# Kernel tuning notes

Hardware: AMD Instinct MI355X
Metric: run time of the kernel (lower is better)

Reference implementation:

```python
import jax, jax.numpy as jnp
import numpy as np

B, D, H, W, C = 4, 8, 16, 16, 512
K_RED = 8
R = C // K_RED          # reduced channels for Q/K
EPS = 1e-3              # keras LayerNormalization default epsilon


def setup_inputs() -> dict:
    key = jax.random.key(0)
    ks = jax.random.split(key, 8)
    s = 0.02
    f32 = jnp.float32
    return {
        "x":  jax.random.normal(ks[0], (B, D, H, W, C), f32),
        # 1x1x1 Conv3D == per-position linear over channels
        "wq": (jax.random.normal(ks[1], (C, R), f32) * s), "bq": jnp.zeros((R,), f32),
        "wk": (jax.random.normal(ks[2], (C, R), f32) * s), "bk": jnp.zeros((R,), f32),
        "wv": (jax.random.normal(ks[3], (C, C), f32) * s), "bv": jnp.zeros((C,), f32),
        "wm": (jax.random.normal(ks[4], (C, C), f32) * s), "bm": jnp.zeros((C,), f32),
        "g1": jnp.ones((C,), f32), "b1": jnp.zeros((C,), f32),
        "g2": jnp.ones((C,), f32), "b2": jnp.zeros((C,), f32),
    }


def _layer_norm(x, g, b):
    m = jnp.mean(x, axis=-1, keepdims=True)
    v = jnp.mean(jnp.square(x - m), axis=-1, keepdims=True)
    return (x - m) * jax.lax.rsqrt(v + EPS) * g + b


def reference(x, wq, bq, wk, bk, wv, bv, wm, bm, g1, b1, g2, b2):
    b, d, h, w, c = x.shape
    f = h * w
    xf = x.reshape(b, d, f, c)                      # [B,D,F,C]
    Q = xf @ wq + bq                                # [B,D,F,R]
    K = xf @ wk + bk                                # [B,D,F,R]
    V = xf @ wv + bv                                # [B,D,F,C]
    # full global scores: [B, D, F, D, F]
    e = jnp.einsum('bifr,bgjr->bifgj', Q, K)
    alphas = jax.nn.softmax(e.reshape(b, d, f, d * f), axis=-1)
    alphas = alphas.reshape(b, d, f, d, f)
    # original einsum 'bdfgh,bdhi->bdfi' sums over key-depth g and uses V at
    # the query depth d; fold the g-sum first, then per-depth F x F matmul.
    a2 = alphas.sum(axis=3)                         # [B,D,F,F]
    attn = jnp.einsum('bdfh,bdhc->bdfc', a2, V)     # [B,D,F,C]
    y1 = _layer_norm(attn + xf, g1, b1)
    y2 = _layer_norm(y1 + jax.nn.relu(y1 @ wm + bm), g2, b2)
    return y2.reshape(b, d, h, w, c)
```

## Files before the change

kernel.cpp:

```cpp
#include <hip/hip_runtime.h>
#include <cstdint>

#define LN_EPS 1e-3f
using u16 = unsigned short;
using u32 = unsigned int;
typedef __attribute__((ext_vector_type(8))) short bh8;
typedef __attribute__((ext_vector_type(4))) float f4;
#define MFMA16(A,B,C) __builtin_amdgcn_mfma_f32_16x16x32_bf16((A),(B),(C),0,0,0)
#define SBAR() __builtin_amdgcn_s_barrier()
#define CFENCE() asm volatile("" ::: "memory")
#define WAITV(N) asm volatile("s_waitcnt vmcnt(" #N ")" ::: "memory")
#define LKBAR() do{ asm volatile("s_waitcnt lgkmcnt(0)" ::: "memory"); \
                    __builtin_amdgcn_s_barrier(); asm volatile("" ::: "memory"); }while(0)

__device__ __forceinline__ u16 bf16r(float f){
    union{float f;u32 u;} c; c.f=f;
    return (u16)((c.u + 0x7fffu + ((c.u>>16)&1u))>>16);
}
__device__ __forceinline__ u32 pk2(float a, float b){
    return (u32)bf16r(a) | ((u32)bf16r(b)<<16);
}
__device__ __forceinline__ void glds16(const void* g, void* l){
    __builtin_amdgcn_global_load_lds(
        (const __attribute__((address_space(1))) u32*)g,
        (__attribute__((address_space(3))) u32*)l, 16, 0, 0);
}

__global__ __launch_bounds__(256) void k0_prep(
    const float* __restrict__ wq, const float* __restrict__ wk,
    const float* __restrict__ wv, const float* __restrict__ wm,
    u16* __restrict__ wqkv_p, u16* __restrict__ wm_p)
{
    const int t = threadIdx.x;
    const int c = t & 15, qn = t >> 4;
    const int quad = qn & 3, ntl = qn >> 2;
    const int blk = blockIdx.x;
    if (blk < 32){
        const int s = blk >> 1, hh = blk & 1;
        const int krow = s*32 + quad*8;
        u16* dst = wqkv_p + (size_t)s*20480;
        #pragma unroll
        for (int i=0;i<5;++i){
            const int nt = hh*20 + i*4 + ntl;
            const int n = nt*16 + c;
            const float* src; int ldw;
            if (n < 64){ src = wq + (size_t)krow*64 + n; ldw = 64; }
            else if (n < 128){ src = wk + (size_t)krow*64 + (n-64); ldw = 64; }
            else { src = wv + (size_t)krow*512 + (n-128); ldw = 512; }
            float v[8];
            #pragma unroll
            for (int j=0;j<8;++j) v[j] = src[(size_t)j*ldw];
            uint4 o; o.x=pk2(v[0],v[1]); o.y=pk2(v[2],v[3]); o.z=pk2(v[4],v[5]); o.w=pk2(v[6],v[7]);
            *(uint4*)&dst[((nt*4+quad)*16 + c)*8] = o;
        }
    } else {
        const int bb = blk - 32;
        const int s = bb >> 1, hh = bb & 1;
        const int krow = s*32 + quad*8;
        u16* dst = wm_p + (size_t)s*16384;
        #pragma unroll
        for (int i=0;i<4;++i){
            const int nt = hh*16 + i*4 + ntl;
            const int n = nt*16 + c;
            const float* src = wm + (size_t)krow*512 + n;
            float v[8];
            #pragma unroll
            for (int j=0;j<8;++j) v[j] = src[(size_t)j*512];
            uint4 o; o.x=pk2(v[0],v[1]); o.y=pk2(v[2],v[3]); o.z=pk2(v[4],v[5]); o.w=pk2(v[6],v[7]);
            *(uint4*)&dst[((nt*4+quad)*16 + c)*8] = o;
        }
    }
}

__global__ __launch_bounds__(512) void k1_qkv(
    const float* __restrict__ x, const float* __restrict__ bq, const float* __restrict__ bk,
    const u16* __restrict__ wqkv_p,
    u16* __restrict__ Qb, u16* __restrict__ Kb, u16* __restrict__ Vb)
{
    __shared__ u16 Asf[16384];
    __shared__ u16 Bs[3][20480];
    const int t = threadIdx.x, w = t>>6, lane = t&63, quad = (lane>>4)&3, c = lane&15;
    const int rg = w>>2, cg = w&3;
    const int rowbase = blockIdx.x << 5;

    #pragma unroll
    for (int i=0;i<5;++i)
        glds16((const char*)wqkv_p + (size_t)w*5120 + i*1024 + lane*16,
               (char*)Bs[0] + w*5120 + i*1024);
    #pragma unroll
    for (int i=0;i<5;++i)
        glds16((const char*)wqkv_p + 40960 + (size_t)w*5120 + i*1024 + lane*16,
               (char*)Bs[1] + w*5120 + i*1024);
    #pragma unroll
    for (int i=0;i<8;++i){
        const int idx = t + (i<<9);
        const int fr = idx >> 7, fc4 = idx & 127;
        float4 xv = *(const float4*)&x[(size_t)(rowbase+fr)*512 + fc4*4];
        uint2 pkv; pkv.x = pk2(xv.x,xv.y); pkv.y = pk2(xv.z,xv.w);
        const int s = fc4 >> 3, qd = (fc4 >> 1) & 3, j0 = (fc4 & 1)*4;
        *(uint2*)&Asf[(fr>>4)*8192 + s*512 + (qd*16 + (fr&15))*8 + j0] = pkv;
    }
    f4 acc[10];
    #pragma unroll
    for (int i=0;i<10;++i) acc[i] = (f4){0.f,0.f,0.f,0.f};
    LKBAR();

    #pragma unroll
    for (int s=0;s<16;++s){
        const u16* Bcur = Bs[s%3];
        bh8 a = *(const bh8*)&Asf[rg*8192 + s*512 + (quad*16+c)*8];
        if (s+2 < 16){
            #pragma unroll
            for (int i=0;i<5;++i)
                glds16((const char*)wqkv_p + (size_t)(s+2)*40960 + (size_t)w*5120 + i*1024 + lane*16,
                       (char*)Bs[(s+2)%3] + w*5120 + i*1024);
            WAITV(10);
        } else if (s+1 < 16){
            WAITV(5);
        } else {
            WAITV(0);
        }
        SBAR(); CFENCE();
        __builtin_amdgcn_s_setprio(1);
        #pragma unroll
        for (int nt2=0;nt2<10;++nt2){
            bh8 bb = *(const bh8*)&Bcur[((cg*10+nt2)*4 + quad)*128 + c*8];
            acc[nt2] = MFMA16(a, bb, acc[nt2]);
        }
        __builtin_amdgcn_s_setprio(0);
        CFENCE(); SBAR();
    }

    const int rt = (blockIdx.x<<1) + rg;
    const int bd = rowbase >> 8;
    const int kloc = (rowbase & 255) + rg*16 + quad*4;
    const int sv = kloc >> 5, kq = (kloc >> 3) & 3, jk0 = kloc & 7;
    #pragma unroll
    for (int nt2=0;nt2<10;++nt2){
        const int colb = cg*160 + nt2*16;
        if (colb < 128){
            const bool isK = (colb >= 64);
            const int r = colb - (isK ? 64 : 0) + c;
            const float bias = isK ? bk[r] : bq[r];
            u16* dstb = (isK ? Kb : Qb) + ((size_t)(rt*2 + (r>>5))*4 + ((r>>3)&3))*128 + (r&7);
            #pragma unroll
            for (int reg=0;reg<4;++reg)
                dstb[(quad*4+reg)*8] = bf16r(acc[nt2][reg] + bias);
        } else {
            const int ntv = (colb - 128) >> 4;
            u16* dstv = Vb + (size_t)bd*131072 + (size_t)sv*16384
                           + (size_t)((ntv*4+kq)*128 + c*8 + jk0);
            ushort4 o;
            o.x = bf16r(acc[nt2][0]); o.y = bf16r(acc[nt2][1]);
            o.z = bf16r(acc[nt2][2]); o.w = bf16r(acc[nt2][3]);
            *(ushort4*)dstv = o;
        }
    }
}

__global__ __launch_bounds__(512) void k234(
    const u16* __restrict__ Qb, const u16* __restrict__ Kb, const u16* __restrict__ Vb,
    const u16* __restrict__ wm_p,
    const float* __restrict__ x, const float* __restrict__ bv,
    const float* __restrict__ g1, const float* __restrict__ b1,
    const float* __restrict__ bm, const float* __restrict__ g2, const float* __restrict__ b2,
    float* __restrict__ out)
{
    __shared__ u16 Bs[3][16384];
    __shared__ u16 y1f[16384];
    __shared__ u16 a2f[8192];
    __shared__ u16 qsf[2048];
    __shared__ float redA[2][4][16], redB[2][4][16];
    const int t = threadIdx.x, w = t>>6, lane = t&63, quad = (lane>>4)&3, c = lane&15;
    const int rg = w>>2, cg = w&3;
    const int bd = blockIdx.x & 31, ftile = blockIdx.x >> 5;
    const int b = bd >> 3;
    const int rowbase = (bd<<8) + (ftile<<5);
    const int rt00 = rowbase >> 4;
    const char* Kbase = (const char*)Kb + (size_t)b*262144;
    const char* Vbase = (const char*)Vb + (size_t)bd*262144;

    if (w < 4) glds16((const char*)Qb + (size_t)rt00*2048 + w*1024 + lane*16,
                      (char*)qsf + w*1024);
    #pragma unroll
    for (int i=0;i<4;++i)
        glds16(Kbase + (size_t)w*4096 + i*1024 + lane*16, (char*)Bs[0] + w*4096 + i*1024);
    #pragma unroll
    for (int i=0;i<4;++i)
        glds16(Kbase + 32768 + (size_t)w*4096 + i*1024 + lane*16, (char*)Bs[1] + w*4096 + i*1024);
    WAITV(8);
    SBAR(); CFENCE();
    bh8 aq0 = *(const bh8*)&qsf[rg*1024 + (quad*16+c)*8];
    bh8 aq1 = *(const bh8*)&qsf[rg*1024 + 512 + (quad*16+c)*8];

    float lp[4] = {0.f,0.f,0.f,0.f};
    float a2r[4][4] = {};
    #pragma unroll
    for (int cc=0; cc<8; ++cc){
        const u16* Bcur = Bs[cc%3];
        if (cc+2 < 8){
            #pragma unroll
            for (int i=0;i<4;++i)
                glds16(Kbase + (size_t)(cc+2)*32768 + (size_t)w*4096 + i*1024 + lane*16,
                       (char*)Bs[(cc+2)%3] + w*4096 + i*1024);
            WAITV(8);
        } else if (cc+1 < 8){
            WAITV(4);
        } else {
            WAITV(0);
        }
        SBAR(); CFENCE();
        __builtin_amdgcn_s_setprio(1);
        f4 sa[4];
        #pragma unroll
        for (int kt=0;kt<4;++kt){
            sa[kt] = (f4){0.f,0.f,0.f,0.f};
            bh8 b0 = *(const bh8*)&Bcur[(cg*4+kt)*1024 + (quad*16+c)*8];
            bh8 bv1= *(const bh8*)&Bcur[(cg*4+kt)*1024 + 512 + (quad*16+c)*8];
            sa[kt] = MFMA16(aq0, b0, sa[kt]);
            sa[kt] = MFMA16(aq1, bv1, sa[kt]);
        }
        __builtin_amdgcn_s_setprio(0);
        #pragma unroll
        for (int kt=0;kt<4;++kt)
            #pragma unroll
            for (int reg=0;reg<4;++reg){
                float e = __expf(sa[kt][reg]);
                lp[reg] += e;
                a2r[reg][kt] += e;
            }
        CFENCE(); SBAR();
    }
    #pragma unroll
    for (int i=0;i<4;++i)
        glds16(Vbase + (size_t)w*4096 + i*1024 + lane*16, (char*)Bs[0] + w*4096 + i*1024);
    #pragma unroll
    for (int i=0;i<4;++i)
        glds16(Vbase + 32768 + (size_t)w*4096 + i*1024 + lane*16, (char*)Bs[1] + w*4096 + i*1024);
    #pragma unroll
    for (int reg=0;reg<4;++reg){
        float v = lp[reg];
        v += __shfl_xor(v,1,64); v += __shfl_xor(v,2,64);
        v += __shfl_xor(v,4,64); v += __shfl_xor(v,8,64);
        lp[reg] = v;
    }
    if (c==0){
        #pragma unroll
        for (int reg=0;reg<4;++reg) redA[rg][cg][quad*4+reg] = lp[reg];
    }
    LKBAR();
    float fac[4];
    #pragma unroll
    for (int reg=0;reg<4;++reg){
        const int q = quad*4+reg;
        fac[reg] = 1.f/(redA[rg][0][q]+redA[rg][1][q]+redA[rg][2][q]+redA[rg][3][q]);
    }
    #pragma unroll
    for (int reg=0;reg<4;++reg)
        #pragma unroll
        for (int kt=0;kt<4;++kt){
            const int jp = cg*64 + kt*16 + c;
            a2f[rg*4096 + (jp>>5)*512 + (((jp>>3)&3)*16 + quad*4+reg)*8 + (jp&7)]
                = bf16r(a2r[reg][kt]*fac[reg]);
        }
    LKBAR();

    f4 cacc[8];
    #pragma unroll
    for (int i=0;i<8;++i) cacc[i] = (f4){0.f,0.f,0.f,0.f};
    #pragma unroll
    for (int s8=0;s8<8;++s8){
        const u16* Bcur = Bs[s8%3];
        bh8 a = *(const bh8*)&a2f[rg*4096 + s8*512 + (quad*16+c)*8];
        if (s8+2 < 8){
            #pragma unroll
            for (int i=0;i<4;++i)
                glds16(Vbase + (size_t)(s8+2)*32768 + (size_t)w*4096 + i*1024 + lane*16,
                       (char*)Bs[(s8+2)%3] + w*4096 + i*1024);
            WAITV(8);
        } else if (s8+1 < 8){
            WAITV(4);
        } else {
            WAITV(0);
        }
        SBAR(); CFENCE();
        __builtin_amdgcn_s_setprio(1);
        #pragma unroll
        for (int nt2=0;nt2<8;++nt2){
            bh8 bb = *(const bh8*)&Bcur[((cg*8+nt2)*4 + quad)*128 + c*8];
            cacc[nt2] = MFMA16(a, bb, cacc[nt2]);
        }
        __builtin_amdgcn_s_setprio(0);
        CFENCE(); SBAR();
    }

    #pragma unroll
    for (int i=0;i<4;++i)
        glds16((const char*)wm_p + (size_t)w*4096 + i*1024 + lane*16,
               (char*)Bs[0] + w*4096 + i*1024);
    #pragma unroll
    for (int i=0;i<4;++i)
        glds16((const char*)wm_p + 32768 + (size_t)w*4096 + i*1024 + lane*16,
               (char*)Bs[1] + w*4096 + i*1024);

    {
        float sv4[4] = {0.f,0.f,0.f,0.f}, qv2[4] = {0.f,0.f,0.f,0.f};
        #pragma unroll
        for (int nt2=0;nt2<8;++nt2){
            const int col = cg*128 + nt2*16 + c;
            const float bvv = bv[col];
            #pragma unroll
            for (int reg=0;reg<4;++reg){
                const int row = rowbase + rg*16 + quad*4 + reg;
                float val = cacc[nt2][reg] + bvv + x[(size_t)row*512 + col];
                cacc[nt2][reg] = val;
                sv4[reg] += val; qv2[reg] = fmaf(val,val,qv2[reg]);
            }
        }
        #pragma unroll
        for (int reg=0;reg<4;++reg){
            float s1=sv4[reg], s2=qv2[reg];
            s1 += __shfl_xor(s1,1,64); s2 += __shfl_xor(s2,1,64);
            s1 += __shfl_xor(s1,2,64); s2 += __shfl_xor(s2,2,64);
            s1 += __shfl_xor(s1,4,64); s2 += __shfl_xor(s2,4,64);
            s1 += __shfl_xor(s1,8,64); s2 += __shfl_xor(s2,8,64);
            sv4[reg]=s1; qv2[reg]=s2;
        }
        if (c==0){
            #pragma unroll
            for (int reg=0;reg<4;++reg){ redA[rg][cg][quad*4+reg]=sv4[reg]; redB[rg][cg][quad*4+reg]=qv2[reg]; }
        }
        LKBAR();
        float mean[4], rstd[4];
        #pragma unroll
        for (int reg=0;reg<4;++reg){
            const int q = quad*4+reg;
            const float S  = redA[rg][0][q]+redA[rg][1][q]+redA[rg][2][q]+redA[rg][3][q];
            const float Q2 = redB[rg][0][q]+redB[rg][1][q]+redB[rg][2][q]+redB[rg][3][q];
            const float m = S*(1.f/512.f);
            mean[reg]=m; rstd[reg]=rsqrtf(Q2*(1.f/512.f) - m*m + LN_EPS);
        }
        #pragma unroll
        for (int nt2=0;nt2<8;++nt2){
            const int col = cg*128 + nt2*16 + c;
            const float gg = g1[col], bb1 = b1[col];
            #pragma unroll
            for (int reg=0;reg<4;++reg){
                float y = (cacc[nt2][reg]-mean[reg])*rstd[reg]*gg + bb1;
                cacc[nt2][reg] = y;
                y1f[rg*8192 + (col>>5)*512 + (((col>>3)&3)*16 + quad*4+reg)*8 + (col&7)] = bf16r(y);
            }
        }
        LKBAR();
    }

    f4 dacc[8];
    #pragma unroll
    for (int i=0;i<8;++i) dacc[i] = (f4){0.f,0.f,0.f,0.f};
    #pragma unroll
    for (int s=0;s<16;++s){
        const u16* Bcur = Bs[s%3];
        bh8 a = *(const bh8*)&y1f[rg*8192 + s*512 + (quad*16+c)*8];
        if (s+2 < 16){
            #pragma unroll
            for (int i=0;i<4;++i)
                glds16((const char*)wm_p + (size_t)(s+2)*32768 + (size_t)w*4096 + i*1024 + lane*16,
                       (char*)Bs[(s+2)%3] + w*4096 + i*1024);
            WAITV(8);
        } else if (s+1 < 16){
            WAITV(4);
        } else {
            WAITV(0);
        }
        SBAR(); CFENCE();
        __builtin_amdgcn_s_setprio(1);
        #pragma unroll
        for (int nt2=0;nt2<8;++nt2){
            bh8 bb = *(const bh8*)&Bcur[((cg*8+nt2)*4 + quad)*128 + c*8];
            dacc[nt2] = MFMA16(a, bb, dacc[nt2]);
        }
        __builtin_amdgcn_s_setprio(0);
        CFENCE(); SBAR();
    }

    {
        float sv4[4] = {0.f,0.f,0.f,0.f}, qv2[4] = {0.f,0.f,0.f,0.f};
        #pragma unroll
        for (int nt2=0;nt2<8;++nt2){
            const int col = cg*128 + nt2*16 + c;
            const float bmv = bm[col];
            #pragma unroll
            for (int reg=0;reg<4;++reg){
                float hh = fmaxf(dacc[nt2][reg]+bmv, 0.f) + cacc[nt2][reg];
                dacc[nt2][reg] = hh;
                sv4[reg] += hh; qv2[reg] = fmaf(hh,hh,qv2[reg]);
            }
        }
        #pragma unroll
        for (int reg=0;reg<4;++reg){
            float s1=sv4[reg], s2=qv2[reg];
            s1 += __shfl_xor(s1,1,64); s2 += __shfl_xor(s2,1,64);
            s1 += __shfl_xor(s1,2,64); s2 += __shfl_xor(s2,2,64);
            s1 += __shfl_xor(s1,4,64); s2 += __shfl_xor(s2,4,64);
            s1 += __shfl_xor(s1,8,64); s2 += __shfl_xor(s2,8,64);
            sv4[reg]=s1; qv2[reg]=s2;
        }
        if (c==0){
            #pragma unroll
            for (int reg=0;reg<4;++reg){ redA[rg][cg][quad*4+reg]=sv4[reg]; redB[rg][cg][quad*4+reg]=qv2[reg]; }
        }
        __syncthreads();
        float mean[4], rstd[4];
        #pragma unroll
        for (int reg=0;reg<4;++reg){
            const int q = quad*4+reg;
            const float S  = redA[rg][0][q]+redA[rg][1][q]+redA[rg][2][q]+redA[rg][3][q];
            const float Q2 = redB[rg][0][q]+redB[rg][1][q]+redB[rg][2][q]+redB[rg][3][q];
            const float m = S*(1.f/512.f);
            mean[reg]=m; rstd[reg]=rsqrtf(Q2*(1.f/512.f) - m*m + LN_EPS);
        }
        #pragma unroll
        for (int nt2=0;nt2<8;++nt2){
            const int col = cg*128 + nt2*16 + c;
            const float gg = g2[col], bb2 = b2[col];
            #pragma unroll
            for (int reg=0;reg<4;++reg){
                const int row = rowbase + rg*16 + quad*4 + reg;
                out[(size_t)row*512 + col] = (dacc[nt2][reg]-mean[reg])*rstd[reg]*gg + bb2;
            }
        }
    }
}

extern "C" void kernel_launch(void* const* d_in, const int* in_sizes, int n_in,
                              void* d_out, int out_size, void* d_ws, size_t ws_size,
                              hipStream_t stream) {
    (void)in_sizes; (void)n_in; (void)out_size; (void)ws_size;
    const float* x  = (const float*)d_in[0];
    const float* wq = (const float*)d_in[1];
    const float* bq = (const float*)d_in[2];
    const float* wk = (const float*)d_in[3];
    const float* bk = (const float*)d_in[4];
    const float* wv = (const float*)d_in[5];
    const float* bv = (const float*)d_in[6];
    const float* wm = (const float*)d_in[7];
    const float* bm = (const float*)d_in[8];
    const float* g1 = (const float*)d_in[9];
    const float* b1 = (const float*)d_in[10];
    const float* g2 = (const float*)d_in[11];
    const float* b2 = (const float*)d_in[12];

    u16* wqkv_p = (u16*)d_ws;
    u16* wm_p   = wqkv_p + 327680;
    u16* Qb     = wm_p   + 262144;
    u16* Kb     = Qb     + 524288;
    u16* Vb     = Kb     + 524288;
    float* outp = (float*)d_out;

    k0_prep<<<64, 256, 0, stream>>>(wq, wk, wv, wm, wqkv_p, wm_p);
    k1_qkv <<<256, 512, 0, stream>>>(x, bq, bk, wqkv_p, Qb, Kb, Vb);
    k234   <<<256, 512, 0, stream>>>(Qb, Kb, Vb, wm_p, x, bv, g1, b1, bm, g2, b2, outp);
}
```

Before: 140.2 us.

## Split k234 into 16-row blocks with double buffering and aliased shared memory

k234 now runs 512 blocks of 256 threads, each handling 16 rows instead of 32. Its triple-buffered shared-memory staging becomes double-buffered, and the q/a2/y1 scratch and reduction buffers are aliased into one region, which cuts LDS per block and should allow more resident blocks. k1's loop is rearranged to wait-then-barrier first and then issue the next prefetch, dropping the trailing barrier. In exchange, each block streams the K/V/Wm tiles for half as many rows, doubling weight and K/V traffic through L2, and the shallower prefetch depth may expose more load latency.

```diff
diff --git a/kernel.cpp b/kernel.cpp
--- a/kernel.cpp
+++ b/kernel.cpp
@@ -107,20 +107,16 @@
 
     #pragma unroll
     for (int s=0;s<16;++s){
-        const u16* Bcur = Bs[s%3];
-        bh8 a = *(const bh8*)&Asf[rg*8192 + s*512 + (quad*16+c)*8];
+        if (s+1 < 16){ WAITV(5); } else { WAITV(0); }
+        SBAR(); CFENCE();
         if (s+2 < 16){
             #pragma unroll
             for (int i=0;i<5;++i)
                 glds16((const char*)wqkv_p + (size_t)(s+2)*40960 + (size_t)w*5120 + i*1024 + lane*16,
                        (char*)Bs[(s+2)%3] + w*5120 + i*1024);
-            WAITV(10);
-        } else if (s+1 < 16){
-            WAITV(5);
-        } else {
-            WAITV(0);
-        }
-        SBAR(); CFENCE();
+        }
+        const u16* Bcur = Bs[s%3];
+        bh8 a = *(const bh8*)&Asf[rg*8192 + s*512 + (quad*16+c)*8];
         __builtin_amdgcn_s_setprio(1);
         #pragma unroll
         for (int nt2=0;nt2<10;++nt2){
@@ -128,7 +124,6 @@
             acc[nt2] = MFMA16(a, bb, acc[nt2]);
         }
         __builtin_amdgcn_s_setprio(0);
-        CFENCE(); SBAR();
     }
 
     const int rt = (blockIdx.x<<1) + rg;
@@ -158,7 +153,7 @@
     }
 }
 
-__global__ __launch_bounds__(512) void k234(
+__global__ __launch_bounds__(256) void k234(
     const u16* __restrict__ Qb, const u16* __restrict__ Kb, const u16* __restrict__ Vb,
     const u16* __restrict__ wm_p,
     const float* __restrict__ x, const float* __restrict__ bv,
@@ -166,50 +161,45 @@
     const float* __restrict__ bm, const float* __restrict__ g2, const float* __restrict__ b2,
     float* __restrict__ out)
 {
-    __shared__ u16 Bs[3][16384];
-    __shared__ u16 y1f[16384];
-    __shared__ u16 a2f[8192];
-    __shared__ u16 qsf[2048];
-    __shared__ float redA[2][4][16], redB[2][4][16];
+    __shared__ u16 Bs[2][16384];
+    __shared__ u16 U[8192];
+    u16* const qsf = U;
+    u16* const a2f = U;
+    u16* const y1f = U;
+    float* const redA = (float*)&U[4096];
+    float* const redB = redA + 64;
     const int t = threadIdx.x, w = t>>6, lane = t&63, quad = (lane>>4)&3, c = lane&15;
-    const int rg = w>>2, cg = w&3;
+    const int cg = w;
     const int bd = blockIdx.x & 31, ftile = blockIdx.x >> 5;
     const int b = bd >> 3;
-    const int rowbase = (bd<<8) + (ftile<<5);
-    const int rt00 = rowbase >> 4;
+    const int rowbase = (bd<<8) + (ftile<<4);
+    const int rt = rowbase >> 4;
     const char* Kbase = (const char*)Kb + (size_t)b*262144;
     const char* Vbase = (const char*)Vb + (size_t)bd*262144;
 
-    if (w < 4) glds16((const char*)Qb + (size_t)rt00*2048 + w*1024 + lane*16,
+    if (w < 2) glds16((const char*)Qb + (size_t)rt*2048 + w*1024 + lane*16,
                       (char*)qsf + w*1024);
     #pragma unroll
-    for (int i=0;i<4;++i)
-        glds16(Kbase + (size_t)w*4096 + i*1024 + lane*16, (char*)Bs[0] + w*4096 + i*1024);
-    #pragma unroll
-    for (int i=0;i<4;++i)
-        glds16(Kbase + 32768 + (size_t)w*4096 + i*1024 + lane*16, (char*)Bs[1] + w*4096 + i*1024);
+    for (int i=0;i<8;++i)
+        glds16(Kbase + (size_t)(w*8+i)*1024 + lane*16, (char*)Bs[0] + (w*8+i)*1024);
     WAITV(8);
     SBAR(); CFENCE();
-    bh8 aq0 = *(const bh8*)&qsf[rg*1024 + (quad*16+c)*8];
-    bh8 aq1 = *(const bh8*)&qsf[rg*1024 + 512 + (quad*16+c)*8];
+    bh8 aq0 = *(const bh8*)&qsf[(quad*16+c)*8];
+    bh8 aq1 = *(const bh8*)&qsf[512 + (quad*16+c)*8];
 
     float lp[4] = {0.f,0.f,0.f,0.f};
     float a2r[4][4] = {};
     #pragma unroll
     for (int cc=0; cc<8; ++cc){
-        const u16* Bcur = Bs[cc%3];
-        if (cc+2 < 8){
-            #pragma unroll
-            for (int i=0;i<4;++i)
-                glds16(Kbase + (size_t)(cc+2)*32768 + (size_t)w*4096 + i*1024 + lane*16,
-                       (char*)Bs[(cc+2)%3] + w*4096 + i*1024);
-            WAITV(8);
-        } else if (cc+1 < 8){
-            WAITV(4);
-        } else {
-            WAITV(0);
-        }
+        WAITV(0);
         SBAR(); CFENCE();
+        if (cc+1 < 8){
+            #pragma unroll
+            for (int i=0;i<8;++i)
+                glds16(Kbase + (size_t)(cc+1)*32768 + (size_t)(w*8+i)*1024 + lane*16,
+                       (char*)Bs[(cc+1)&1] + (w*8+i)*1024);
+        }
+        const u16* Bcur = Bs[cc&1];
         __builtin_amdgcn_s_setprio(1);
         f4 sa[4];
         #pragma unroll
@@ -229,14 +219,10 @@
                 lp[reg] += e;
                 a2r[reg][kt] += e;
             }
-        CFENCE(); SBAR();
-    }
-    #pragma unroll
-    for (int i=0;i<4;++i)
-        glds16(Vbase + (size_t)w*4096 + i*1024 + lane*16, (char*)Bs[0] + w*4096 + i*1024);
-    #pragma unroll
-    for (int i=0;i<4;++i)
-        glds16(Vbase + 32768 + (size_t)w*4096 + i*1024 + lane*16, (char*)Bs[1] + w*4096 + i*1024);
+    }
+    #pragma unroll
+    for (int i=0;i<8;++i)
+        glds16(Vbase + (size_t)(w*8+i)*1024 + lane*16, (char*)Bs[0] + (w*8+i)*1024);
     #pragma unroll
     for (int reg=0;reg<4;++reg){
         float v = lp[reg];
@@ -246,21 +232,24 @@
     }
     if (c==0){
         #pragma unroll
-        for (int reg=0;reg<4;++reg) redA[rg][cg][quad*4+reg] = lp[reg];
+        for (int reg=0;reg<4;++reg) redA[cg*16 + quad*4+reg] = lp[reg];
     }
     LKBAR();
+    #pragma unroll
+    for (int i=0;i<8;++i)
+        glds16(Vbase + 32768 + (size_t)(w*8+i)*1024 + lane*16, (char*)Bs[1] + (w*8+i)*1024);
     float fac[4];
     #pragma unroll
     for (int reg=0;reg<4;++reg){
         const int q = quad*4+reg;
-        fac[reg] = 1.f/(redA[rg][0][q]+redA[rg][1][q]+redA[rg][2][q]+redA[rg][3][q]);
+        fac[reg] = 1.f/(redA[q]+redA[16+q]+redA[32+q]+redA[48+q]);
     }
     #pragma unroll
     for (int reg=0;reg<4;++reg)
         #pragma unroll
         for (int kt=0;kt<4;++kt){
             const int jp = cg*64 + kt*16 + c;
-            a2f[rg*4096 + (jp>>5)*512 + (((jp>>3)&3)*16 + quad*4+reg)*8 + (jp&7)]
+            a2f[(jp>>5)*512 + (((jp>>3)&3)*16 + quad*4+reg)*8 + (jp&7)]
                 = bf16r(a2r[reg][kt]*fac[reg]);
         }
     LKBAR();
@@ -270,20 +259,16 @@
     for (int i=0;i<8;++i) cacc[i] = (f4){0.f,0.f,0.f,0.f};
     #pragma unroll
     for (int s8=0;s8<8;++s8){
-        const u16* Bcur = Bs[s8%3];
-        bh8 a = *(const bh8*)&a2f[rg*4096 + s8*512 + (quad*16+c)*8];
-        if (s8+2 < 8){
-            #pragma unroll
-            for (int i=0;i<4;++i)
-                glds16(Vbase + (size_t)(s8+2)*32768 + (size_t)w*4096 + i*1024 + lane*16,
-                       (char*)Bs[(s8+2)%3] + w*4096 + i*1024);
-            WAITV(8);
-        } else if (s8+1 < 8){
-            WAITV(4);
-        } else {
-            WAITV(0);
-        }
+        if (s8==0){ WAITV(8); } else { WAITV(0); }
         SBAR(); CFENCE();
+        if (s8>=1 && s8+1<8){
+            #pragma unroll
+            for (int i=0;i<8;++i)
+                glds16(Vbase + (size_t)(s8+1)*32768 + (size_t)(w*8+i)*1024 + lane*16,
+                       (char*)Bs[(s8+1)&1] + (w*8+i)*1024);
+        }
+        const u16* Bcur = Bs[s8&1];
+        bh8 a = *(const bh8*)&a2f[s8*512 + (quad*16+c)*8];
         __builtin_amdgcn_s_setprio(1);
         #pragma unroll
         for (int nt2=0;nt2<8;++nt2){
@@ -291,17 +276,11 @@
             cacc[nt2] = MFMA16(a, bb, cacc[nt2]);
         }
         __builtin_amdgcn_s_setprio(0);
-        CFENCE(); SBAR();
-    }
-
-    #pragma unroll
-    for (int i=0;i<4;++i)
-        glds16((const char*)wm_p + (size_t)w*4096 + i*1024 + lane*16,
-               (char*)Bs[0] + w*4096 + i*1024);
-    #pragma unroll
-    for (int i=0;i<4;++i)
-        glds16((const char*)wm_p + 32768 + (size_t)w*4096 + i*1024 + lane*16,
-               (char*)Bs[1] + w*4096 + i*1024);
+    }
+    #pragma unroll
+    for (int i=0;i<8;++i)
+        glds16((const char*)wm_p + (size_t)(w*8+i)*1024 + lane*16,
+               (char*)Bs[0] + (w*8+i)*1024);
 
     {
         float sv4[4] = {0.f,0.f,0.f,0.f}, qv2[4] = {0.f,0.f,0.f,0.f};
@@ -311,7 +290,7 @@
             const float bvv = bv[col];
             #pragma unroll
             for (int reg=0;reg<4;++reg){
-                const int row = rowbase + rg*16 + quad*4 + reg;
+                const int row = rowbase + quad*4 + reg;
                 float val = cacc[nt2][reg] + bvv + x[(size_t)row*512 + col];
                 cacc[nt2][reg] = val;
                 sv4[reg] += val; qv2[reg] = fmaf(val,val,qv2[reg]);
@@ -328,18 +307,23 @@
         }
         if (c==0){
             #pragma unroll
-            for (int reg=0;reg<4;++reg){ redA[rg][cg][quad*4+reg]=sv4[reg]; redB[rg][cg][quad*4+reg]=qv2[reg]; }
+            for (int reg=0;reg<4;++reg){ redA[cg*16+quad*4+reg]=sv4[reg]; redB[cg*16+quad*4+reg]=qv2[reg]; }
         }
         LKBAR();
+        #pragma unroll
+        for (int i=0;i<8;++i)
+            glds16((const char*)wm_p + 32768 + (size_t)(w*8+i)*1024 + lane*16,
+                   (char*)Bs[1] + (w*8+i)*1024);
         float mean[4], rstd[4];
         #pragma unroll
         for (int reg=0;reg<4;++reg){
             const int q = quad*4+reg;
-            const float S  = redA[rg][0][q]+redA[rg][1][q]+redA[rg][2][q]+redA[rg][3][q];
-            const float Q2 = redB[rg][0][q]+redB[rg][1][q]+redB[rg][2][q]+redB[rg][3][q];
+            const float S  = redA[q]+redA[16+q]+redA[32+q]+redA[48+q];
+            const float Q2 = redB[q]+redB[16+q]+redB[32+q]+redB[48+q];
             const float m = S*(1.f/512.f);
             mean[reg]=m; rstd[reg]=rsqrtf(Q2*(1.f/512.f) - m*m + LN_EPS);
         }
+        SBAR(); CFENCE();
         #pragma unroll
         for (int nt2=0;nt2<8;++nt2){
             const int col = cg*128 + nt2*16 + c;
@@ -348,7 +332,7 @@
             for (int reg=0;reg<4;++reg){
                 float y = (cacc[nt2][reg]-mean[reg])*rstd[reg]*gg + bb1;
                 cacc[nt2][reg] = y;
-                y1f[rg*8192 + (col>>5)*512 + (((col>>3)&3)*16 + quad*4+reg)*8 + (col&7)] = bf16r(y);
+                y1f[(col>>5)*512 + (((col>>3)&3)*16 + quad*4+reg)*8 + (col&7)] = bf16r(y);
             }
         }
         LKBAR();
@@ -359,20 +343,16 @@
     for (int i=0;i<8;++i) dacc[i] = (f4){0.f,0.f,0.f,0.f};
     #pragma unroll
     for (int s=0;s<16;++s){
-        const u16* Bcur = Bs[s%3];
-        bh8 a = *(const bh8*)&y1f[rg*8192 + s*512 + (quad*16+c)*8];
-        if (s+2 < 16){
-            #pragma unroll
-            for (int i=0;i<4;++i)
-                glds16((const char*)wm_p + (size_t)(s+2)*32768 + (size_t)w*4096 + i*1024 + lane*16,
-                       (char*)Bs[(s+2)%3] + w*4096 + i*1024);
-            WAITV(8);
-        } else if (s+1 < 16){
-            WAITV(4);
-        } else {
-            WAITV(0);
-        }
+        if (s==0){ WAITV(8); } else { WAITV(0); }
         SBAR(); CFENCE();
+        if (s>=1 && s+1<16){
+            #pragma unroll
+            for (int i=0;i<8;++i)
+                glds16((const char*)wm_p + (size_t)(s+1)*32768 + (size_t)(w*8+i)*1024 + lane*16,
+                       (char*)Bs[(s+1)&1] + (w*8+i)*1024);
+        }
+        const u16* Bcur = Bs[s&1];
+        bh8 a = *(const bh8*)&y1f[s*512 + (quad*16+c)*8];
         __builtin_amdgcn_s_setprio(1);
         #pragma unroll
         for (int nt2=0;nt2<8;++nt2){
@@ -380,7 +360,6 @@
             dacc[nt2] = MFMA16(a, bb, dacc[nt2]);
         }
         __builtin_amdgcn_s_setprio(0);
-        CFENCE(); SBAR();
     }
 
     {
@@ -407,15 +386,15 @@
         }
         if (c==0){
             #pragma unroll
-            for (int reg=0;reg<4;++reg){ redA[rg][cg][quad*4+reg]=sv4[reg]; redB[rg][cg][quad*4+reg]=qv2[reg]; }
-        }
-        __syncthreads();
+            for (int reg=0;reg<4;++reg){ redA[cg*16+quad*4+reg]=sv4[reg]; redB[cg*16+quad*4+reg]=qv2[reg]; }
+        }
+        LKBAR();
         float mean[4], rstd[4];
         #pragma unroll
         for (int reg=0;reg<4;++reg){
             const int q = quad*4+reg;
-            const float S  = redA[rg][0][q]+redA[rg][1][q]+redA[rg][2][q]+redA[rg][3][q];
-            const float Q2 = redB[rg][0][q]+redB[rg][1][q]+redB[rg][2][q]+redB[rg][3][q];
+            const float S  = redA[q]+redA[16+q]+redA[32+q]+redA[48+q];
+            const float Q2 = redB[q]+redB[16+q]+redB[32+q]+redB[48+q];
             const float m = S*(1.f/512.f);
             mean[reg]=m; rstd[reg]=rsqrtf(Q2*(1.f/512.f) - m*m + LN_EPS);
         }
@@ -425,7 +404,7 @@
             const float gg = g2[col], bb2 = b2[col];
             #pragma unroll
             for (int reg=0;reg<4;++reg){
-                const int row = rowbase + rg*16 + quad*4 + reg;
+                const int row = rowbase + quad*4 + reg;
                 out[(size_t)row*512 + col] = (dacc[nt2][reg]-mean[reg])*rstd[reg]*gg + bb2;
             }
         }
@@ -459,5 +438,5 @@
 
     k0_prep<<<64, 256, 0, stream>>>(wq, wk, wv, wm, wqkv_p, wm_p);
     k1_qkv <<<256, 512, 0, stream>>>(x, bq, bk, wqkv_p, Qb, Kb, Vb);
-    k234   <<<256, 512, 0, stream>>>(Qb, Kb, Vb, wm_p, x, bv, g1, b1, bm, g2, b2, outp);
-}
+    k234   <<<512, 256, 0, stream>>>(Qb, Kb, Vb, wm_p, x, bv, g1, b1, bm, g2, b2, outp);
+}
```

Measured after the change: 162.2 us. 15.7% more time.
